# Performance work log

Measured on AMD Instinct MI355X. Metric: run time of the kernel, lower is better.

Reference implementation:

```python
import jax, jax.numpy as jnp
import numpy as np

B, C, CO, N = 2, 32, 32, 64
MODES, LMAX, RBINS = 16, 2, 16
HALF = MODES // 2
NL = (LMAX + 1) ** 2  # 9 real spherical harmonics up to l=2
M = MODES ** 3
HID = 16  # round(CO * 0.5)


def _build_basis():
    # frequencies of the kept FNO corner modes along each axis
    f = np.concatenate([np.arange(HALF), np.arange(-HALF, 0)]).astype(np.float32)
    kx, ky, kz = np.meshgrid(f, f, f, indexing='ij')
    kx, ky, kz = kx.ravel(), ky.ravel(), kz.ravel()
    r = np.sqrt(kx ** 2 + ky ** 2 + kz ** 2)
    nzm = (r > 0).astype(np.float32)
    inv = np.where(r > 0, 1.0 / np.maximum(r, 1e-9), 0.0)
    ux, uy, uz = kx * inv, ky * inv, kz * inv
    # real spherical harmonics l=0,1,2 (cartesian form); all l>0 vanish at DC
    Y = np.stack([
        0.282095 * np.ones_like(r),
        0.488603 * uy, 0.488603 * uz, 0.488603 * ux,
        1.092548 * ux * uy, 1.092548 * uy * uz,
        0.315392 * (3.0 * uz ** 2 - nzm),
        1.092548 * ux * uz, 0.546274 * (ux ** 2 - uy ** 2)], axis=0)  # [NL, M]
    shell = np.minimum((r / (r.max() + 1e-6) * RBINS).astype(np.int64), RBINS - 1)
    cnt = np.bincount(shell, minlength=RBINS).astype(np.float32)
    w = 1.0 / np.sqrt(np.maximum(cnt, 1.0))
    mask = (shell[None, :] == np.arange(RBINS)[:, None]).astype(np.float32) * w[:, None]  # [RBINS, M]
    return (mask[:, None, :] * Y[None]).reshape(RBINS * NL, M).astype(np.float32)

BASIS = jnp.asarray(_build_basis())  # [K=144, M=4096], fixed projection basis
IDX = jnp.asarray(np.concatenate([np.arange(HALF), np.arange(N - HALF, N)]))  # kept mode indices


def cgelu(z):
    return jax.nn.gelu(z.real) + 1j * jax.nn.gelu(z.imag)


def setup_inputs() -> dict:
    key = jax.random.key(0)
    ks = jax.random.split(key, 17)
    rn = lambda k, s: jax.random.normal(k, s, dtype=jnp.float32)
    return {
        'x': rn(ks[0], (B, C, N, N, N)),
        'w_fno_r': rn(ks[1], (CO, C)) * 0.1, 'w_fno_i': rn(ks[2], (CO, C)) * 0.1,
        'b_fno_r': rn(ks[3], (CO,)) * 0.1, 'b_fno_i': rn(ks[4], (CO,)) * 0.1,
        'w_gate_r': rn(ks[5], (CO,)), 'w_gate_i': rn(ks[6], (CO,)),
        'w_spec_r': rn(ks[7], (RBINS, NL, C, CO)) * 0.1, 'w_spec_i': rn(ks[8], (RBINS, NL, C, CO)) * 0.1,
        'mlp_w1_r': rn(ks[9], (HID, CO)) * 0.1, 'mlp_w1_i': rn(ks[10], (HID, CO)) * 0.1,
        'mlp_b1_r': rn(ks[11], (HID,)) * 0.1, 'mlp_b1_i': rn(ks[12], (HID,)) * 0.1,
        'mlp_w2_r': rn(ks[13], (CO, HID)) * 0.1, 'mlp_w2_i': rn(ks[14], (CO, HID)) * 0.1,
        'mlp_b2_r': rn(ks[15], (CO,)) * 0.1, 'mlp_b2_i': rn(ks[16], (CO,)) * 0.1,
    }


def reference(x, w_fno_r, w_fno_i, b_fno_r, b_fno_i, w_gate_r, w_gate_i,
              w_spec_r, w_spec_i, mlp_w1_r, mlp_w1_i, mlp_b1_r, mlp_b1_i,
              mlp_w2_r, mlp_w2_i, mlp_b2_r, mlp_b2_i):
    cx = lambda r, i: (r + 1j * i).astype(jnp.complex64)
    xc = x.astype(jnp.complex64)
    w_fno, b_fno = cx(w_fno_r, w_fno_i), cx(b_fno_r, b_fno_i)
    w_gate = cx(w_gate_r, w_gate_i)
    w_spec = cx(w_spec_r, w_spec_i)
    w1, b1 = cx(mlp_w1_r, mlp_w1_i), cx(mlp_b1_r, mlp_b1_i)
    w2, b2 = cx(mlp_w2_r, mlp_w2_i), cx(mlp_b2_r, mlp_b2_i)

    # skip paths: complex 1x1-conv ('linear') and complex soft-gating
    skip_fno = jnp.einsum('oc,bcxyz->boxyz', w_fno, xc) + b_fno[None, :, None, None, None]
    skip_mlp = xc * w_gate[None, :, None, None, None]

    # Harmonic layer: FFT -> slice kept modes -> harmonic/radial projection
    # -> complex spectral conv -> inverse projection -> scatter -> iFFT
    xf = jnp.fft.fftn(xc, axes=(-3, -2, -1))
    xs = xf[:, :, IDX[:, None, None], IDX[None, :, None], IDX[None, None, :]].reshape(B, C, M)
    coeffs = jnp.einsum('bcm,km->bck', xs, BASIS).reshape(B, C, RBINS, NL)
    coeffs = jnp.einsum('bisl,slio->bosl', coeffs, w_spec)
    xs2 = jnp.einsum('bck,km->bcm', coeffs.reshape(B, CO, RBINS * NL), BASIS)
    full = jnp.zeros((B, CO, N, N, N), jnp.complex64).at[
        :, :, IDX[:, None, None], IDX[None, :, None], IDX[None, None, :]
    ].set(xs2.reshape(B, CO, MODES, MODES, MODES))
    x_fno = jnp.fft.ifftn(full, axes=(-3, -2, -1))

    x1 = x_fno + skip_fno  # n_layers=1 -> no activation here
    h = cgelu(jnp.einsum('hc,bcxyz->bhxyz', w1, x1) + b1[None, :, None, None, None])
    y = jnp.einsum('oh,bhxyz->boxyz', w2, h) + b2[None, :, None, None, None]
    return (y + skip_mlp).real
```

## Files before the change

### kernel.cpp

```cpp
#include <hip/hip_runtime.h>
#include <hip/hip_bf16.h>

#define PI2 6.283185307179586f

typedef __attribute__((ext_vector_type(8))) short short8;
typedef __attribute__((ext_vector_type(4))) float f32x4;

static const size_t O_Y      = 0;
static const size_t O_W1RT   = 36864;
static const size_t O_W1IT   = 37376;
static const size_t O_W1XR   = 37888;
static const size_t O_W1XI   = 38400;
static const size_t O_B1PR   = 38912;
static const size_t O_B1PI   = 38928;
static const size_t O_WSH    = 38944;
static const size_t O_SHELL  = 38960;
static const size_t O_ORDER  = 43056;
static const size_t O_SSTART = 47152;
static const size_t O_COEF   = 47232;
static const size_t O_COEF2  = 65664;
static const size_t O_XS     = 84096;
static const size_t O_FRAG   = 608384;
static const size_t O_TWF    = 616576;
static const size_t O_TWB    = 617088;
static const size_t O_FRG12  = 617600;
static const size_t O_T2     = 1132672;
static const size_t O_T1     = 3229824;

static __device__ __forceinline__ float geluf(float v) {
  float e = __expf(-1.702f * v);
  return v / (1.0f + e);
}

static __device__ __forceinline__ unsigned int f2bfbits(float f) {
  unsigned int u = __float_as_uint(f);
  u += 0x7fffu + ((u >> 16) & 1u);
  return u >> 16;
}

static __device__ __forceinline__ unsigned int pk2(float a, float b) {
  return f2bfbits(a) | (f2bfbits(b) << 16);
}

__global__ __launch_bounds__(256) void k0_init(
    const float* __restrict__ wfr, const float* __restrict__ wfi,
    const float* __restrict__ bfr, const float* __restrict__ bfi,
    const float* __restrict__ w1r, const float* __restrict__ w1i,
    const float* __restrict__ b1r, const float* __restrict__ b1i,
    const float* __restrict__ w2r, const float* __restrict__ w2i,
    float* __restrict__ ws) {
  float* Y    = ws + O_Y;
  float* w1rt = ws + O_W1RT;  float* w1it = ws + O_W1IT;
  float* W1xr = ws + O_W1XR;  float* W1xi = ws + O_W1XI;
  float* b1pr = ws + O_B1PR;  float* b1pi = ws + O_B1PI;
  float* wsh  = ws + O_WSH;
  int* shellOf = (int*)(ws + O_SHELL);
  int* order   = (int*)(ws + O_ORDER);
  int* sstart  = (int*)(ws + O_SSTART);

  __shared__ int cnt[16], fill[16], st[17];
  int tid = threadIdx.x;
  if (tid < 16) { cnt[tid] = 0; fill[tid] = 0; }
  __syncthreads();
  for (int m = tid; m < 4096; m += 256) {
    int ix = m >> 8, iy = (m >> 4) & 15, iz = m & 15;
    float kx = (float)(ix < 8 ? ix : ix - 16);
    float ky = (float)(iy < 8 ? iy : iy - 16);
    float kz = (float)(iz < 8 ? iz : iz - 16);
    float r2 = kx*kx + ky*ky + kz*kz;
    float r  = sqrtf(r2);
    float nzm = r2 > 0.f ? 1.f : 0.f;
    float inv = r2 > 0.f ? 1.0f / fmaxf(r, 1e-9f) : 0.f;
    float ux = kx*inv, uy = ky*inv, uz = kz*inv;
    Y[0*4096+m] = 0.282095f;
    Y[1*4096+m] = 0.488603f * uy;
    Y[2*4096+m] = 0.488603f * uz;
    Y[3*4096+m] = 0.488603f * ux;
    Y[4*4096+m] = 1.092548f * ux*uy;
    Y[5*4096+m] = 1.092548f * uy*uz;
    Y[6*4096+m] = 0.315392f * (3.0f*uz*uz - nzm);
    Y[7*4096+m] = 1.092548f * ux*uz;
    Y[8*4096+m] = 0.546274f * (ux*ux - uy*uy);
    float rmax = sqrtf(192.0f);
    float t = r / (rmax + 1e-6f) * 16.0f;
    int sh = (int)t; sh = sh > 15 ? 15 : sh;
    shellOf[m] = sh;
    atomicAdd(&cnt[sh], 1);
  }
  __syncthreads();
  if (tid == 0) { int a = 0; for (int s = 0; s < 16; ++s) { st[s] = a; a += cnt[s]; } st[16] = a; }
  __syncthreads();
  if (tid < 16) wsh[tid] = 1.0f / sqrtf(fmaxf((float)cnt[tid], 1.0f));
  if (tid < 17) sstart[tid] = st[tid];
  for (int m = tid; m < 4096; m += 256) {
    int sh = shellOf[m];
    int p = atomicAdd(&fill[sh], 1);
    order[st[sh] + p] = m;
  }
  for (int e = tid; e < 512; e += 256) {
    int j = e >> 5, c = e & 31;
    float ar = 0.f, ai = 0.f;
    for (int o = 0; o < 32; ++o) {
      float wr_ = w1r[j*32+o], wi_ = w1i[j*32+o];
      float fr  = wfr[o*32+c], fi_ = wfi[o*32+c];
      ar += wr_*fr - wi_*fi_;
      ai += wr_*fi_ + wi_*fr;
    }
    W1xr[c*16+j] = ar;  W1xi[c*16+j] = ai;
    w1rt[c*16+j] = w1r[j*32+c];
    w1it[c*16+j] = w1i[j*32+c];
  }
  if (tid < 16) {
    int j = tid;
    float ar = b1r[j], ai = b1i[j];
    for (int o = 0; o < 32; ++o) {
      ar += w1r[j*32+o]*bfr[o] - w1i[j*32+o]*bfi[o];
      ai += w1r[j*32+o]*bfi[o] + w1i[j*32+o]*bfr[o];
    }
    b1pr[j] = ar; b1pi[j] = ai;
  }

  {
    int k = tid >> 4, i2 = tid & 15;
    float fk = (float)(k < 8 ? k : k - 16);
    float s, c;
    __sincosf(-PI2 * fk * (float)i2 / 64.0f, &s, &c);
    ((float2*)(ws + O_TWF))[tid] = make_float2(c, s);
    int g = tid >> 4, kk = tid & 15;
    float fkk = (float)(kk < 8 ? kk : kk - 16);
    __sincosf(PI2 * fkk * (float)g / 64.0f, &s, &c);
    ((float2*)(ws + O_TWB))[tid] = make_float2(c, s);
  }
  if (tid < 64) {
    unsigned int* fp12 = (unsigned int*)(ws + O_FRG12) + tid*16;
    int p = tid & 15, q = tid >> 4;
    float fp_ = (float)(p < 8 ? p : p - 16);
    #pragma unroll
    for (int ch = 0; ch < 2; ++ch) {
      float cj[8], sj[8];
      #pragma unroll
      for (int j = 0; j < 8; ++j) {
        int z = ch*32 + 8*q + j;
        float s, c; __sincosf(-PI2 * fp_ * (float)z / 64.0f, &s, &c);
        cj[j] = c; sj[j] = s;
      }
      #pragma unroll
      for (int s2 = 0; s2 < 4; ++s2) {
        fp12[ch*8 + s2]     = pk2(cj[2*s2], cj[2*s2+1]);
        fp12[ch*8 + 4 + s2] = pk2(sj[2*s2], sj[2*s2+1]);
      }
    }
  }
  __syncthreads();

  {
    unsigned int* fp = (unsigned int*)(ws + O_FRAG) + tid*32;
    int lane = tid & 63, wvv = tid >> 6;
    int p = lane & 15, q = lane >> 4;
    int z = wvv*16 + p;
    float arj[8], aij[8];
    #pragma unroll
    for (int j = 0; j < 8; ++j) {
      int k = 8*q + j;
      int kz = k & 15;
      float f = (float)(kz < 8 ? kz : kz - 16);
      float s, c; __sincosf(PI2 * f * (float)z / 64.0f, &s, &c);
      arj[j] = (k < 16) ? c : -s;
      aij[j] = (k < 16) ? s : c;
    }
    #pragma unroll
    for (int s2 = 0; s2 < 4; ++s2) {
      fp[s2]     = pk2(arj[2*s2], arj[2*s2+1]);
      fp[4 + s2] = pk2(aij[2*s2], aij[2*s2+1]);
    }
    #pragma unroll
    for (int s = 0; s < 4; ++s) {
      int c0 = 8*q + 2*s, c1 = c0 + 1;
      fp[8  + s] = pk2(w1rt[c0*16 + p], w1rt[c1*16 + p]);
      fp[12 + s] = pk2(w1it[c0*16 + p], w1it[c1*16 + p]);
      fp[16 + s] = pk2(W1xr[c0*16 + p], W1xr[c1*16 + p]);
      fp[20 + s] = pk2(W1xi[c0*16 + p], W1xi[c1*16 + p]);
    }
    #pragma unroll
    for (int mt = 0; mt < 2; ++mt) {
      int o = mt*16 + p;
      #pragma unroll
      for (int s = 0; s < 4; ++s) {
        int kk = 8*q + 2*s;
        float a  = (kk   < 16) ? w2r[o*16 + kk]      : -w2i[o*16 + kk - 16];
        float bb = (kk+1 < 16) ? w2r[o*16 + kk + 1]  : -w2i[o*16 + kk - 15];
        fp[24 + mt*4 + s] = pk2(a, bb);
      }
    }
  }
}

__global__ __launch_bounds__(256) void k12_fwd(const float* __restrict__ x,
    const float* __restrict__ ws, float* __restrict__ T2) {
  __shared__ __align__(16) float us[2592];
  __shared__ float2 slab[64*17];
  __hip_bfloat16* xT = (__hip_bfloat16*)us;
  float* ysum = us;
  int blk = blockIdx.x;
  const float* src = x + (size_t)blk * 4096;
  int tid = threadIdx.x;
  int lane = tid & 63, wv = tid >> 6;
  int p = lane & 15, q = lane >> 4;

  union U8 { short8 v; unsigned int u[4]; };

  U8 fc0, fs0, fc1, fs1;
  {
    const uint4* f12 = (const uint4*)(ws + O_FRG12) + (size_t)lane*4;
    uint4 a0 = f12[0], a1 = f12[1], a2 = f12[2], a3 = f12[3];
    fc0.u[0]=a0.x; fc0.u[1]=a0.y; fc0.u[2]=a0.z; fc0.u[3]=a0.w;
    fs0.u[0]=a1.x; fs0.u[1]=a1.y; fs0.u[2]=a1.z; fs0.u[3]=a1.w;
    fc1.u[0]=a2.x; fc1.u[1]=a2.y; fc1.u[2]=a2.z; fc1.u[3]=a2.w;
    fs1.u[0]=a3.x; fs1.u[1]=a3.y; fs1.u[2]=a3.z; fs1.u[3]=a3.w;
  }

  for (int i = tid; i < 1024; i += 256) {
    int y = i >> 4, zq = i & 15;
    float4 v = *(const float4*)&src[y*64 + 4*zq];
    int rb = y*72 + 4*zq;
    xT[rb]   = __float2bfloat16(v.x);
    xT[rb+1] = __float2bfloat16(v.y);
    xT[rb+2] = __float2bfloat16(v.z);
    xT[rb+3] = __float2bfloat16(v.w);
  }
  __syncthreads();

  {
    U8 b0, b1;
    const __hip_bfloat16* xrow = &xT[(wv*16 + p)*72];
    *(uint4*)&b0.u[0] = *(const uint4*)&xrow[8*q];
    *(uint4*)&b1.u[0] = *(const uint4*)&xrow[32 + 8*q];
    f32x4 zac = {0.f, 0.f, 0.f, 0.f};
    f32x4 Dr = __builtin_amdgcn_mfma_f32_16x16x32_bf16(fc0.v, b0.v, zac, 0, 0, 0);
    Dr       = __builtin_amdgcn_mfma_f32_16x16x32_bf16(fc1.v, b1.v, Dr,  0, 0, 0);
    f32x4 Di = __builtin_amdgcn_mfma_f32_16x16x32_bf16(fs0.v, b0.v, zac, 0, 0, 0);
    Di       = __builtin_amdgcn_mfma_f32_16x16x32_bf16(fs1.v, b1.v, Di,  0, 0, 0);
    __syncthreads();
    #pragma unroll
    for (int r = 0; r < 4; ++r)
      slab[(wv*16 + p)*17 + 4*q + r] = make_float2(Dr[r], Di[r]);
  }
  __syncthreads();

  {
    int y0 = tid >> 4, kz = tid & 15;
    float2 u0 = slab[(y0     )*17 + kz];
    float2 u1 = slab[(y0 + 16)*17 + kz];
    float2 u2 = slab[(y0 + 32)*17 + kz];
    float2 u3 = slab[(y0 + 48)*17 + kz];
    float Ar = u0.x + u2.x, Ai = u0.y + u2.y;
    float Br = u0.x - u2.x, Bi = u0.y - u2.y;
    float Cr = u1.x + u3.x, Ci = u1.y + u3.y;
    float Dr = u1.x - u3.x, Di = u1.y - u3.y;
    float* yp = ysum + y0*162 + kz*10;
    yp[0] = Ar + Cr;  yp[1] = Ai + Ci;
    yp[2] = Br + Di;  yp[3] = Bi - Dr;
    yp[4] = Ar - Cr;  yp[5] = Ai - Ci;
    yp[6] = Br - Di;  yp[7] = Bi + Dr;
  }
  __syncthreads();

  {
    int kz = tid & 15, kyi = tid >> 4;
    const float* yp = ysum + kz*10 + (kyi & 3)*2;
    const float2* twp = (const float2*)(ws + O_TWF) + kyi*16;
    float ar = 0.f, ai = 0.f;
    #pragma unroll
    for (int y0 = 0; y0 < 16; ++y0) {
      float sr = yp[y0*162], si = yp[y0*162 + 1];
      float2 w = twp[y0];
      ar += sr*w.x - si*w.y;
      ai += sr*w.y + si*w.x;
    }
    *(float2*)&T2[(size_t)blk*512 + (kyi*16 + kz)*2] = make_float2(ar, ai);
  }
}

__global__ __launch_bounds__(256) void k3_dftx(const float* __restrict__ T2,
    const float* __restrict__ ws, float* __restrict__ xs) {
  __shared__ float slab[64*34];
  __shared__ float xsum[2592];
  int blk = blockIdx.x;
  int bc = blk >> 4, ky = blk & 15;
  int tid = threadIdx.x;
  for (int i = tid; i < 2048; i += 256) {
    int xr = i >> 5, rem = i & 31;
    slab[xr*34 + rem] = T2[((size_t)(bc*64 + xr)*16 + ky)*32 + rem];
  }
  __syncthreads();
  {
    int x0 = tid >> 4, kz = tid & 15;
    const float2* sp = (const float2*)slab;
    float2 u0 = sp[(x0     )*17 + kz];
    float2 u1 = sp[(x0 + 16)*17 + kz];
    float2 u2 = sp[(x0 + 32)*17 + kz];
    float2 u3 = sp[(x0 + 48)*17 + kz];
    float Ar = u0.x + u2.x, Ai = u0.y + u2.y;
    float Br = u0.x - u2.x, Bi = u0.y - u2.y;
    float Cr = u1.x + u3.x, Ci = u1.y + u3.y;
    float Dr = u1.x - u3.x, Di = u1.y - u3.y;
    float* yp = xsum + x0*162 + kz*10;
    yp[0] = Ar + Cr;  yp[1] = Ai + Ci;
    yp[2] = Br + Di;  yp[3] = Bi - Dr;
    yp[4] = Ar - Cr;  yp[5] = Ai - Ci;
    yp[6] = Br - Di;  yp[7] = Bi + Dr;
  }
  __syncthreads();
  {
    int kz = tid & 15, kxi = tid >> 4;
    const float* yp = xsum + kz*10 + (kxi & 3)*2;
    const float2* twp = (const float2*)(ws + O_TWF) + kxi*16;
    float ar = 0.f, ai = 0.f;
    #pragma unroll
    for (int x0 = 0; x0 < 16; ++x0) {
      float sr = yp[x0*162], si = yp[x0*162 + 1];
      float2 w = twp[x0];
      ar += sr*w.x - si*w.y;
      ai += sr*w.y + si*w.x;
    }
    *(float2*)&xs[(size_t)bc*8192 + (kxi*256 + ky*16 + kz)*2] = make_float2(ar, ai);
  }
}

__global__ __launch_bounds__(256) void k4_proj(const float* __restrict__ xs, const float* __restrict__ Y,
    const int* __restrict__ order, const int* __restrict__ sstart, const float* __restrict__ wsh,
    float* __restrict__ coeffs) {
  int blk = blockIdx.x; int bc = blk >> 4, s = blk & 15;
  int tid = threadIdx.x;
  int st = sstart[s], en = sstart[s+1];
  float ar[9], ai[9];
  #pragma unroll
  for (int l = 0; l < 9; ++l) { ar[l] = 0.f; ai[l] = 0.f; }
  for (int ii = st + tid; ii < en; ii += 256) {
    int m = order[ii];
    float2 v = *(const float2*)&xs[(size_t)bc*8192 + m*2];
    #pragma unroll
    for (int l = 0; l < 9; ++l) {
      float yv = Y[l*4096 + m];
      ar[l] += yv * v.x; ai[l] += yv * v.y;
    }
  }
  #pragma unroll
  for (int l = 0; l < 9; ++l) {
    #pragma unroll
    for (int d = 1; d < 64; d <<= 1) {
      ar[l] += __shfl_xor(ar[l], d, 64);
      ai[l] += __shfl_xor(ai[l], d, 64);
    }
  }
  __shared__ float wred[4][18];
  int wv = tid >> 6, lane = tid & 63;
  if (lane == 0) {
    #pragma unroll
    for (int l = 0; l < 9; ++l) { wred[wv][l] = ar[l]; wred[wv][9 + l] = ai[l]; }
  }
  __syncthreads();
  if (tid < 18) {
    float sum = wred[0][tid] + wred[1][tid] + wred[2][tid] + wred[3][tid];
    float w = wsh[s];
    int l = tid < 9 ? tid : tid - 9;
    int ri = tid < 9 ? 0 : 1;
    coeffs[((size_t)bc*144 + s*9 + l)*2 + ri] = w * sum;
  }
}

__global__ __launch_bounds__(256) void k5_spec(const float* __restrict__ coeffs,
    const float* __restrict__ wsr, const float* __restrict__ wsi, float* __restrict__ coeffs2) {
  int item = blockIdx.x * 8 + (threadIdx.x >> 5);
  int b = item / 144, sl = item - b * 144;
  int o = threadIdx.x & 31;
  float ar = 0.f, ai = 0.f;
  for (int i = 0; i < 32; ++i) {
    float cr = coeffs[((size_t)(b*32 + i)*144 + sl)*2];
    float ci = coeffs[((size_t)(b*32 + i)*144 + sl)*2 + 1];
    float wr = wsr[(sl*32 + i)*32 + o];
    float wi = wsi[(sl*32 + i)*32 + o];
    ar += cr*wr - ci*wi;
    ai += cr*wi + ci*wr;
  }
  const float sc = 1.0f / 262144.0f;
  coeffs2[((size_t)(b*32 + o)*144 + sl)*2]     = ar * sc;
  coeffs2[((size_t)(b*32 + o)*144 + sl)*2 + 1] = ai * sc;
}

__global__ __launch_bounds__(256) void k78(const float* __restrict__ coeffs2,
    const float* __restrict__ Y, const int* __restrict__ shellOf, const float* __restrict__ wsh,
    const float* __restrict__ twb, float* __restrict__ U1) {
  __shared__ float c2[288];
  __shared__ float slab[512];
  int blk = blockIdx.x;
  int bo = blk >> 4, ky = blk & 15;
  int tid = threadIdx.x;

  for (int i = tid; i < 288; i += 256) c2[i] = coeffs2[(size_t)bo*288 + i];
  __syncthreads();

  {
    int kxi = tid >> 4, kz = tid & 15;
    int m = kxi*256 + ky*16 + kz;
    int sh = shellOf[m];
    float w = wsh[sh];
    float ar = 0.f, ai = 0.f;
    #pragma unroll
    for (int l = 0; l < 9; ++l) {
      float yv = Y[l*4096 + m];
      ar += yv * c2[(sh*9 + l)*2];
      ai += yv * c2[(sh*9 + l)*2 + 1];
    }
    slab[tid*2]     = w * ar;
    slab[tid*2 + 1] = w * ai;
  }
  __syncthreads();

  int kz = tid & 15, grp = tid >> 4;
  const float2* tb = (const float2*)twb + grp*16;
  float sjr[4] = {0.f,0.f,0.f,0.f}, sji[4] = {0.f,0.f,0.f,0.f};
  #pragma unroll
  for (int kx = 0; kx < 16; ++kx) {
    float2 w = tb[kx];
    float2 v = *(const float2*)&slab[(kx*16 + kz)*2];
    sjr[kx & 3] += v.x*w.x - v.y*w.y;
    sji[kx & 3] += v.x*w.y + v.y*w.x;
  }
  float Ar = sjr[0]+sjr[2], Ai = sji[0]+sji[2];
  float Br = sjr[0]-sjr[2], Bi = sji[0]-sji[2];
  float Cr = sjr[1]+sjr[3], Ci = sji[1]+sji[3];
  float Dr = sjr[1]-sjr[3], Di = sji[1]-sji[3];
  *(float2*)&U1[((size_t)(bo*64 + grp     )*16 + ky)*32 + kz*2] = make_float2(Ar+Cr, Ai+Ci);
  *(float2*)&U1[((size_t)(bo*64 + grp + 16)*16 + ky)*32 + kz*2] = make_float2(Br-Di, Bi+Dr);
  *(float2*)&U1[((size_t)(bo*64 + grp + 32)*16 + ky)*32 + kz*2] = make_float2(Ar-Cr, Ai-Ci);
  *(float2*)&U1[((size_t)(bo*64 + grp + 48)*16 + ky)*32 + kz*2] = make_float2(Br+Di, Bi-Dr);
}

__global__ __launch_bounds__(256) void k9_invy(const float* __restrict__ U1,
    const float* __restrict__ twb, float* __restrict__ U2) {
  __shared__ float slab[512];
  int blk = blockIdx.x;
  int tid = threadIdx.x;
  const float* src = U1 + (size_t)blk * 512;
  for (int i = tid; i < 512; i += 256) slab[i] = src[i];
  __syncthreads();
  int kz = tid & 15, grp = tid >> 4;
  const float2* tb = (const float2*)twb + grp*16;
  float sjr[4] = {0.f,0.f,0.f,0.f}, sji[4] = {0.f,0.f,0.f,0.f};
  #pragma unroll
  for (int ky = 0; ky < 16; ++ky) {
    float2 w = tb[ky];
    float2 v = *(const float2*)&slab[(ky*16 + kz)*2];
    sjr[ky & 3] += v.x*w.x - v.y*w.y;
    sji[ky & 3] += v.x*w.y + v.y*w.x;
  }
  float Ar = sjr[0]+sjr[2], Ai = sji[0]+sji[2];
  float Br = sjr[0]-sjr[2], Bi = sji[0]-sji[2];
  float Cr = sjr[1]+sjr[3], Ci = sji[1]+sji[3];
  float Dr = sjr[1]-sjr[3], Di = sji[1]-sji[3];
  float* dst = U2 + (size_t)blk * 2048;
  *(float2*)&dst[((grp     )*16 + kz)*2] = make_float2(Ar+Cr, Ai+Ci);
  *(float2*)&dst[((grp + 16)*16 + kz)*2] = make_float2(Br-Di, Bi+Dr);
  *(float2*)&dst[((grp + 32)*16 + kz)*2] = make_float2(Ar-Cr, Ai-Ci);
  *(float2*)&dst[((grp + 48)*16 + kz)*2] = make_float2(Br+Di, Bi-Dr);
}

__global__ __launch_bounds__(256) void k10_final(
    const float* __restrict__ x, const float* __restrict__ U2,
    const float* __restrict__ ws,
    const float* __restrict__ b2r, const float* __restrict__ wgr,
    float* __restrict__ out) {
  const float* b1pr = ws + O_B1PR;  const float* b1pi = ws + O_B1PI;

  __shared__ unsigned int xfT[128*33];
  __shared__ __hip_bfloat16 xlT[128*34];
  __shared__ f32x4 hpW4[272];
  unsigned int* hpW = (unsigned int*)hpW4;
  unsigned int* Bt  = (unsigned int*)hpW4;

  int tid = threadIdx.x;
  int blk = blockIdx.x;
  int yb = blk & 31, bx = blk >> 5;
  int b = bx >> 6, xr = bx & 63;
  int y0 = yb * 2;

  int lane = tid & 63, wv = tid >> 6;
  int p = lane & 15, q = lane >> 4;

  union U8 { short8 v; unsigned int u[4]; };

  const uint4* fpt = (const uint4*)(ws + O_FRAG) + (size_t)tid * 8;
  U8 fAr, fAi;
  {
    uint4 a0 = fpt[0], a1 = fpt[1];
    fAr.u[0]=a0.x; fAr.u[1]=a0.y; fAr.u[2]=a0.z; fAr.u[3]=a0.w;
    fAi.u[0]=a1.x; fAi.u[1]=a1.y; fAi.u[2]=a1.z; fAi.u[3]=a1.w;
  }

  for (int i = tid; i < 1024; i += 256) {
    int ya = i >> 9, c = (i >> 4) & 31, zq = i & 15;
    const float4 v = *(const float4*)&x[(size_t)(b*32 + c)*262144 + (size_t)xr*4096
                                        + (size_t)(y0 + ya)*64 + 4*zq];
    int rb = ((ya << 6) + 4*zq)*34 + c;
    xlT[rb]       = __float2bfloat16(v.x);
    xlT[rb + 34]  = __float2bfloat16(v.y);
    xlT[rb + 68]  = __float2bfloat16(v.z);
    xlT[rb + 102] = __float2bfloat16(v.w);
  }
  {
    int ya = tid >> 7, o = (tid >> 2) & 31, t4 = tid & 3;
    const float4* g4 = (const float4*)(U2 + ((size_t)((b*32 + o)*64 + xr))*2048
                                       + (size_t)(y0 + ya)*32 + 8*t4);
    float4 ga = g4[0], gb = g4[1];
    unsigned int* bp = Bt + (ya*32 + o)*17;
    bp[2*t4]         = pk2(ga.x, ga.z);
    bp[2*t4 + 1]     = pk2(gb.x, gb.z);
    bp[8 + 2*t4]     = pk2(ga.y, ga.w);
    bp[8 + 2*t4 + 1] = pk2(gb.y, gb.w);
  }
  __syncthreads();

  {
    f32x4 zac = {0.f, 0.f, 0.f, 0.f};
    #pragma unroll
    for (int ya = 0; ya < 2; ++ya) {
      #pragma unroll
      for (int ot = 0; ot < 2; ++ot) {
        U8 fB;
        uint4 bv = *(const uint4*)(Bt + (ya*32 + ot*16 + p)*17 + 4*q);
        fB.u[0] = bv.x; fB.u[1] = bv.y; fB.u[2] = bv.z; fB.u[3] = bv.w;
        f32x4 Dr = __builtin_amdgcn_mfma_f32_16x16x32_bf16(fAr.v, fB.v, zac, 0, 0, 0);
        f32x4 Di = __builtin_amdgcn_mfma_f32_16x16x32_bf16(fAi.v, fB.v, zac, 0, 0, 0);
        int rowb = ya*64 + wv*16 + 4*q;
        #pragma unroll
        for (int r = 0; r < 4; ++r)
          xfT[(rowb + r)*33 + ot*16 + p] = pk2(Dr[r], Di[r]);
      }
    }
  }
  __syncthreads();

  {
    int wb = wv * 272;

    U8 fW1r, fW1i, fW1iN, fW1xr, fW1xi, fW2[2];
    {
      uint4 b0 = fpt[2], b1 = fpt[3], b2v = fpt[4], b3 = fpt[5], b4 = fpt[6], b5 = fpt[7];
      fW1r.u[0]=b0.x;  fW1r.u[1]=b0.y;  fW1r.u[2]=b0.z;  fW1r.u[3]=b0.w;
      fW1i.u[0]=b1.x;  fW1i.u[1]=b1.y;  fW1i.u[2]=b1.z;  fW1i.u[3]=b1.w;
      fW1xr.u[0]=b2v.x; fW1xr.u[1]=b2v.y; fW1xr.u[2]=b2v.z; fW1xr.u[3]=b2v.w;
      fW1xi.u[0]=b3.x; fW1xi.u[1]=b3.y; fW1xi.u[2]=b3.z; fW1xi.u[3]=b3.w;
      fW2[0].u[0]=b4.x; fW2[0].u[1]=b4.y; fW2[0].u[2]=b4.z; fW2[0].u[3]=b4.w;
      fW2[1].u[0]=b5.x; fW2[1].u[1]=b5.y; fW2[1].u[2]=b5.z; fW2[1].u[3]=b5.w;
      #pragma unroll
      for (int s = 0; s < 4; ++s) fW1iN.u[s] = fW1i.u[s] ^ 0x80008000u;
    }
    float4 b1r4 = *(const float4*)(b1pr + 4*q);
    float4 b1i4 = *(const float4*)(b1pi + 4*q);
    float b2a[2][4], wga[2][4];
    #pragma unroll
    for (int mt = 0; mt < 2; ++mt) {
      float4 t0 = *(const float4*)(b2r + mt*16 + 4*q);
      float4 t1 = *(const float4*)(wgr + mt*16 + 4*q);
      b2a[mt][0]=t0.x; b2a[mt][1]=t0.y; b2a[mt][2]=t0.z; b2a[mt][3]=t0.w;
      wga[mt][0]=t1.x; wga[mt][1]=t1.y; wga[mt][2]=t1.z; wga[mt][3]=t1.w;
    }
    float b1ra[4] = {b1r4.x, b1r4.y, b1r4.z, b1r4.w};
    float b1ia[4] = {b1i4.x, b1i4.y, b1i4.z, b1i4.w};

    f32x4 zacc = {0.f, 0.f, 0.f, 0.f};
    const unsigned int* xlW = (const unsigned int*)xlT;

    for (int tt = 0; tt < 2; ++tt) {
      int tile = wv*2 + tt;
      int ya = tile >> 2, zg = tile & 3;
      int row = ya*64 + zg*16 + p;

      unsigned int w8[8];
      #pragma unroll
      for (int jj = 0; jj < 8; ++jj) w8[jj] = xfT[row*33 + 8*q + jj];
      U8 FR, FI, XV;
      #pragma unroll
      for (int s = 0; s < 4; ++s) {
        FR.u[s] = __builtin_amdgcn_perm(w8[2*s+1], w8[2*s], 0x05040100u);
        FI.u[s] = __builtin_amdgcn_perm(w8[2*s+1], w8[2*s], 0x07060302u);
        XV.u[s] = xlW[row*17 + 4*q + s];
      }

      f32x4 accR = zacc, accI = zacc;
      accR = __builtin_amdgcn_mfma_f32_16x16x32_bf16(fW1r.v,  FR.v, accR, 0, 0, 0);
      accR = __builtin_amdgcn_mfma_f32_16x16x32_bf16(fW1iN.v, FI.v, accR, 0, 0, 0);
      accR = __builtin_amdgcn_mfma_f32_16x16x32_bf16(fW1xr.v, XV.v, accR, 0, 0, 0);
      accI = __builtin_amdgcn_mfma_f32_16x16x32_bf16(fW1r.v,  FI.v, accI, 0, 0, 0);
      accI = __builtin_amdgcn_mfma_f32_16x16x32_bf16(fW1i.v,  FR.v, accI, 0, 0, 0);
      accI = __builtin_amdgcn_mfma_f32_16x16x32_bf16(fW1xi.v, XV.v, accI, 0, 0, 0);

      float hr_[4], hi_[4];
      #pragma unroll
      for (int r = 0; r < 4; ++r) {
        hr_[r] = geluf(accR[r] + b1ra[r]);
        hi_[r] = geluf(accI[r] + b1ia[r]);
      }
      hpW[wb + 17*p + 2*q]     = pk2(hr_[0], hr_[1]);
      hpW[wb + 17*p + 2*q + 1] = pk2(hr_[2], hr_[3]);
      hpW[wb + 17*p + 8 + 2*q]     = pk2(hi_[0], hi_[1]);
      hpW[wb + 17*p + 8 + 2*q + 1] = pk2(hi_[2], hi_[3]);

      U8 FH;
      #pragma unroll
      for (int s = 0; s < 4; ++s) FH.u[s] = hpW[wb + 17*p + 4*q + s];

      #pragma unroll
      for (int mt = 0; mt < 2; ++mt) {
        f32x4 accO = __builtin_amdgcn_mfma_f32_16x16x32_bf16(fW2[mt].v, FH.v, zacc, 0, 0, 0);
        #pragma unroll
        for (int r = 0; r < 4; ++r) {
          int o = mt*16 + q*4 + r;
          int z = zg*16 + p;
          float xv = __bfloat162float(xlT[row*34 + o]);
          out[(size_t)(b*32 + o)*262144 + (size_t)xr*4096 + (size_t)(y0 + ya)*64 + z]
              = accO[r] + b2a[mt][r] + wga[mt][r]*xv;
        }
      }
    }
  }
}

extern "C" void kernel_launch(void* const* d_in, const int* in_sizes, int n_in,
                              void* d_out, int out_size, void* d_ws, size_t ws_size,
                              hipStream_t stream) {
  (void)in_sizes; (void)n_in; (void)out_size; (void)ws_size;
  const float* x   = (const float*)d_in[0];
  const float* wfr = (const float*)d_in[1];
  const float* wfi = (const float*)d_in[2];
  const float* bfr = (const float*)d_in[3];
  const float* bfi = (const float*)d_in[4];
  const float* wgr = (const float*)d_in[5];
  const float* wsr = (const float*)d_in[7];
  const float* wsi = (const float*)d_in[8];
  const float* w1r = (const float*)d_in[9];
  const float* w1i = (const float*)d_in[10];
  const float* b1r = (const float*)d_in[11];
  const float* b1i = (const float*)d_in[12];
  const float* w2r = (const float*)d_in[13];
  const float* w2i = (const float*)d_in[14];
  const float* b2r = (const float*)d_in[15];
  float* out = (float*)d_out;
  float* ws  = (float*)d_ws;

  float* T1      = ws + O_T1;
  float* T2      = ws + O_T2;
  float* xs      = ws + O_XS;
  float* coeffs  = ws + O_COEF;
  float* coeffs2 = ws + O_COEF2;
  float* Y       = ws + O_Y;
  int* shellOf   = (int*)(ws + O_SHELL);
  int* order     = (int*)(ws + O_ORDER);
  int* sstart    = (int*)(ws + O_SSTART);
  float* wsh     = ws + O_WSH;
  float* twb     = ws + O_TWB;

  hipLaunchKernelGGL(k0_init,  dim3(1),    dim3(256), 0, stream, wfr, wfi, bfr, bfi, w1r, w1i, b1r, b1i, w2r, w2i, ws);
  hipLaunchKernelGGL(k12_fwd,  dim3(4096), dim3(256), 0, stream, x, ws, T2);
  hipLaunchKernelGGL(k3_dftx,  dim3(1024), dim3(256), 0, stream, T2, ws, xs);
  hipLaunchKernelGGL(k4_proj,  dim3(1024), dim3(256), 0, stream, xs, Y, order, sstart, wsh, coeffs);
  hipLaunchKernelGGL(k5_spec,  dim3(36),   dim3(256), 0, stream, coeffs, wsr, wsi, coeffs2);
  hipLaunchKernelGGL(k78,      dim3(1024), dim3(256), 0, stream, coeffs2, Y, shellOf, wsh, twb, T2);
  hipLaunchKernelGGL(k9_invy,  dim3(4096), dim3(256), 0, stream, T2, twb, T1);
  hipLaunchKernelGGL(k10_final,dim3(4096), dim3(256), 0, stream, x, T1, ws, b2r, wgr, out);
}
```

Baseline: 238.3 us.

## Fuse x-axis DFT with harmonic projection via shared-memory atomic reduction

Merges the x-axis DFT kernel and the harmonic/radial projection kernel into one. Each thread now weights its own mode by its shell's Y values and accumulates into a shared-memory coefficient table with atomics. The table is then added to global coefficients with global atomics, which requires k0_init to zero the coefficient buffer. This drops one launch and the round trip of the intermediate mode array through global memory, at the cost of heavy LDS atomic contention and non-deterministic float summation order.

```diff
diff --git a/kernel.cpp b/kernel.cpp
--- a/kernel.cpp
+++ b/kernel.cpp
@@ -19,7 +19,6 @@
 static const size_t O_SSTART = 47152;
 static const size_t O_COEF   = 47232;
 static const size_t O_COEF2  = 65664;
-static const size_t O_XS     = 84096;
 static const size_t O_FRAG   = 608384;
 static const size_t O_TWF    = 616576;
 static const size_t O_TWB    = 617088;
@@ -62,6 +61,7 @@
   int tid = threadIdx.x;
   if (tid < 16) { cnt[tid] = 0; fill[tid] = 0; }
   __syncthreads();
+  for (int i = tid; i < 18432; i += 256) (ws + O_COEF)[i] = 0.f;
   for (int m = tid; m < 4096; m += 256) {
     int ix = m >> 8, iy = (m >> 4) & 15, iz = m & 15;
     float kx = (float)(ix < 8 ? ix : ix - 16);
@@ -281,13 +281,18 @@
   }
 }
 
-__global__ __launch_bounds__(256) void k3_dftx(const float* __restrict__ T2,
-    const float* __restrict__ ws, float* __restrict__ xs) {
+__global__ __launch_bounds__(256) void k34_dftx_proj(const float* __restrict__ T2,
+    const float* __restrict__ ws, float* __restrict__ coeffs) {
+  const float* Y = ws + O_Y;
+  const int* shellOf = (const int*)(ws + O_SHELL);
+  const float* wsh = ws + O_WSH;
   __shared__ float slab[64*34];
   __shared__ float xsum[2592];
+  __shared__ float cred[288];
   int blk = blockIdx.x;
   int bc = blk >> 4, ky = blk & 15;
   int tid = threadIdx.x;
+  for (int i = tid; i < 288; i += 256) cred[i] = 0.f;
   for (int i = tid; i < 2048; i += 256) {
     int xr = i >> 5, rem = i & 31;
     slab[xr*34 + rem] = T2[((size_t)(bc*64 + xr)*16 + ky)*32 + rem];
@@ -323,49 +328,21 @@
       ar += sr*w.x - si*w.y;
       ai += sr*w.y + si*w.x;
     }
-    *(float2*)&xs[(size_t)bc*8192 + (kxi*256 + ky*16 + kz)*2] = make_float2(ar, ai);
-  }
-}
-
-__global__ __launch_bounds__(256) void k4_proj(const float* __restrict__ xs, const float* __restrict__ Y,
-    const int* __restrict__ order, const int* __restrict__ sstart, const float* __restrict__ wsh,
-    float* __restrict__ coeffs) {
-  int blk = blockIdx.x; int bc = blk >> 4, s = blk & 15;
-  int tid = threadIdx.x;
-  int st = sstart[s], en = sstart[s+1];
-  float ar[9], ai[9];
-  #pragma unroll
-  for (int l = 0; l < 9; ++l) { ar[l] = 0.f; ai[l] = 0.f; }
-  for (int ii = st + tid; ii < en; ii += 256) {
-    int m = order[ii];
-    float2 v = *(const float2*)&xs[(size_t)bc*8192 + m*2];
+    int m = kxi*256 + ky*16 + kz;
+    int sh = shellOf[m];
+    float w = wsh[sh];
+    float war = w * ar, wai = w * ai;
     #pragma unroll
     for (int l = 0; l < 9; ++l) {
       float yv = Y[l*4096 + m];
-      ar[l] += yv * v.x; ai[l] += yv * v.y;
-    }
-  }
-  #pragma unroll
-  for (int l = 0; l < 9; ++l) {
-    #pragma unroll
-    for (int d = 1; d < 64; d <<= 1) {
-      ar[l] += __shfl_xor(ar[l], d, 64);
-      ai[l] += __shfl_xor(ai[l], d, 64);
-    }
-  }
-  __shared__ float wred[4][18];
-  int wv = tid >> 6, lane = tid & 63;
-  if (lane == 0) {
-    #pragma unroll
-    for (int l = 0; l < 9; ++l) { wred[wv][l] = ar[l]; wred[wv][9 + l] = ai[l]; }
-  }
-  __syncthreads();
-  if (tid < 18) {
-    float sum = wred[0][tid] + wred[1][tid] + wred[2][tid] + wred[3][tid];
-    float w = wsh[s];
-    int l = tid < 9 ? tid : tid - 9;
-    int ri = tid < 9 ? 0 : 1;
-    coeffs[((size_t)bc*144 + s*9 + l)*2 + ri] = w * sum;
+      atomicAdd(&cred[(sh*9 + l)*2],     yv * war);
+      atomicAdd(&cred[(sh*9 + l)*2 + 1], yv * wai);
+    }
+  }
+  __syncthreads();
+  for (int i = tid; i < 288; i += 256) {
+    float v = cred[i];
+    if (v != 0.f) atomicAdd(&coeffs[(size_t)bc*288 + i], v);
   }
 }
 
@@ -651,20 +628,16 @@
 
   float* T1      = ws + O_T1;
   float* T2      = ws + O_T2;
-  float* xs      = ws + O_XS;
   float* coeffs  = ws + O_COEF;
   float* coeffs2 = ws + O_COEF2;
   float* Y       = ws + O_Y;
   int* shellOf   = (int*)(ws + O_SHELL);
-  int* order     = (int*)(ws + O_ORDER);
-  int* sstart    = (int*)(ws + O_SSTART);
   float* wsh     = ws + O_WSH;
   float* twb     = ws + O_TWB;
 
   hipLaunchKernelGGL(k0_init,  dim3(1),    dim3(256), 0, stream, wfr, wfi, bfr, bfi, w1r, w1i, b1r, b1i, w2r, w2i, ws);
   hipLaunchKernelGGL(k12_fwd,  dim3(4096), dim3(256), 0, stream, x, ws, T2);
-  hipLaunchKernelGGL(k3_dftx,  dim3(1024), dim3(256), 0, stream, T2, ws, xs);
-  hipLaunchKernelGGL(k4_proj,  dim3(1024), dim3(256), 0, stream, xs, Y, order, sstart, wsh, coeffs);
+  hipLaunchKernelGGL(k34_dftx_proj, dim3(1024), dim3(256), 0, stream, T2, ws, coeffs);
   hipLaunchKernelGGL(k5_spec,  dim3(36),   dim3(256), 0, stream, coeffs, wsr, wsi, coeffs2);
   hipLaunchKernelGGL(k78,      dim3(1024), dim3(256), 0, stream, coeffs2, Y, shellOf, wsh, twb, T2);
   hipLaunchKernelGGL(k9_invy,  dim3(4096), dim3(256), 0, stream, T2, twb, T1);
```

Result: slower. 257.5 us (+8.1%).
